# Kernel optimization log

Hardware: AMD Instinct MI355X
Metric: run time of the kernel (lower is better)

## Reference

```python
import jax, jax.numpy as jnp
import numpy as np

BS, MA, H, NH = 64, 64, 64, 4  # molecules, max atoms per molecule, hsize, n_heads


def _lengths():
    # deterministic ragged molecule sizes in [24, 64]
    return np.array([24 + (7 * i) % 41 for i in range(BS)], dtype=np.int64)


def _scopes():
    lengths = _lengths()
    N = int(lengths.sum())  # 2774
    scope = np.zeros((BS, MA), dtype=np.int64)      # pad slots gather row 0 (zeros)
    rev = np.zeros((N,), dtype=np.int64)            # flat atom -> b*MA + slot
    pos = 1                                          # flat row 0 is the zero pad row
    for b, L in enumerate(lengths):
        scope[b, :L] = np.arange(pos, pos + L)
        rev[pos - 1:pos - 1 + L] = b * MA + np.arange(L)
        pos += L
    return scope, rev, N


def setup_inputs() -> dict:
    key = jax.random.key(0)
    k0, k1, k2, k3 = jax.random.split(key, 4)
    scope, rev, N = _scopes()
    inputs = jax.random.normal(k0, (N + 1, H), dtype=jnp.float32)
    inputs = inputs.at[0].set(0.0)  # zero pad row, as in graphretro flat tensors
    Wa_pair = jax.random.normal(k1, (H, H * NH), dtype=jnp.float32) * (1.0 / np.sqrt(H))
    Wa_score = jax.random.normal(k2, (H, NH), dtype=jnp.float32) * (1.0 / np.sqrt(H))
    W_proj = jax.random.normal(k3, (H * NH, H), dtype=jnp.float32) * (1.0 / np.sqrt(H * NH))
    return {
        "inputs": inputs,
        "scope_tensor": jnp.asarray(scope),
        "scope_rev_tensor": jnp.asarray(rev),
        "Wa_pair": Wa_pair,
        "Wa_score": Wa_score,
        "W_proj": W_proj,
    }


def reference(inputs, scope_tensor, scope_rev_tensor, Wa_pair, Wa_score, W_proj):
    bs, ma = scope_tensor.shape
    h = inputs.shape[1]
    nh = Wa_score.shape[1]
    # flat_to_batch: [bs, ma, h]; pad slots pull the zero row 0
    c_batch = inputs[scope_tensor]
    # get_pair: pairwise sum of atom embeddings -> [bs, ma, ma, h]
    atom_pair = c_batch[:, :, None, :] + c_batch[:, None, :, :]
    # Wa_pair (no bias) + relu, viewed as [bs, ma, ma, h, nh]
    total_att = jax.nn.relu(atom_pair @ Wa_pair).reshape(bs, ma, ma, h, nh)
    # einsum '...hn,hjn->...jn' with j==1, then sigmoid -> [bs, ma, ma, nh]
    att_score = jax.nn.sigmoid(jnp.einsum('bijhn,hn->bijn', total_att, Wa_score))
    # att_score * c_atom[b,j,h], summed over j -> [bs, ma, h, nh]
    c_sum = jnp.einsum('bijn,bjh->bihn', att_score, c_batch)
    # view to [bs, ma, h*nh] (h-major, matching torch .view) and project
    c_atom_att = c_sum.reshape(bs, ma, h * nh) @ W_proj  # [bs, ma, h]
    c_mol_att = c_atom_att.sum(axis=1)  # [bs, h]
    # batch_to_flat + prepend zero row -> [N+1, h]
    flat = c_atom_att.reshape(bs * ma, h)[scope_rev_tensor]
    c_atom_att_flat = jnp.concatenate([jnp.zeros((1, h), flat.dtype), flat], axis=0)
    return (c_mol_att, c_atom_att_flat)
```

## Files before the change

### kernel.cpp

```cpp
#include <hip/hip_runtime.h>
#include <stdint.h>

typedef _Float16 h2 __attribute__((ext_vector_type(2)));
typedef _Float16 h8 __attribute__((ext_vector_type(8)));
typedef float f32x4 __attribute__((ext_vector_type(4)));
typedef unsigned int u32;
typedef unsigned short u16;

#define WT_STR 68
#define PJ_STR 68
#define WP_STR 268
#define PI_STR 36
#define CB_STR 72
#define CT_STR 68
#define AB_STR 72
#define CS_STR 264
#define WS_STR 36

__device__ __forceinline__ u32 pk2(float a, float b) {
    return __builtin_bit_cast(u32, __builtin_amdgcn_cvt_pkrtz(a, b));
}
__device__ __forceinline__ h8 frag4(u32 a, u32 b, u32 c, u32 d) {
    return __builtin_bit_cast(h8, make_uint4(a, b, c, d));
}

__global__ __launch_bounds__(512, 1) void atom_attn(
    const float* __restrict__ inputs,
    const int*   __restrict__ scope,
    const float* __restrict__ Wa_pair,
    const float* __restrict__ Wa_score,
    const float* __restrict__ W_proj,
    float* __restrict__ out_mol,
    float* __restrict__ out_flat)
{
    __shared__ __align__(16) u16 s_wa[256 * WT_STR];
    __shared__ __align__(16) u16 s_pj[256 * PJ_STR];
    __shared__ __align__(16) u16 s_wp[64 * WP_STR];
    __shared__ __align__(16) u32 s_pi[4 * 16 * PI_STR];
    __shared__ __align__(16) u16 s_cb[64 * CB_STR];
    __shared__ __align__(16) u16 s_ct[64 * CT_STR];
    __shared__ __align__(16) u16 s_ab[64 * AB_STR];
    __shared__ __align__(16) u16 s_cs[16 * CS_STR];
    __shared__ __align__(16) u32 s_ws[4 * WS_STR];

    const int t = threadIdx.x;
    const int w = t >> 6, l = t & 63;
    const int ml = l & 15, q = l >> 4;
    const int b = blockIdx.y, bx = blockIdx.x;
    const int i_base = bx * 16;

    if (t < 256) {
        if (t < 128) {
            const int n = t & 3, hh = t >> 2;
            const float g0 = Wa_score[(2 * hh) * 4 + n];
            const float g1 = Wa_score[(2 * hh + 1) * 4 + n];
            s_ws[n * WS_STR + hh] = pk2(g0, g1);
        }
        {
            const int jp = (t & 31) * 2;
            const int pp = t >> 5;
            const int r0 = scope[b * 64 + jp];
            const int r1 = scope[b * 64 + jp + 1];
            const f32x4 a0 = *(const f32x4*)(inputs + (size_t)r0 * 64 + pp * 8);
            const f32x4 a1 = *(const f32x4*)(inputs + (size_t)r0 * 64 + pp * 8 + 4);
            const f32x4 b0 = *(const f32x4*)(inputs + (size_t)r1 * 64 + pp * 8);
            const f32x4 b1 = *(const f32x4*)(inputs + (size_t)r1 * 64 + pp * 8 + 4);
            float A[8] = {a0[0], a0[1], a0[2], a0[3], a1[0], a1[1], a1[2], a1[3]};
            float B[8] = {b0[0], b0[1], b0[2], b0[3], b1[0], b1[1], b1[2], b1[3]};
            *(uint4*)&s_cb[jp * CB_STR + pp * 8] =
                make_uint4(pk2(A[0], A[1]), pk2(A[2], A[3]), pk2(A[4], A[5]), pk2(A[6], A[7]));
            *(uint4*)&s_cb[(jp + 1) * CB_STR + pp * 8] =
                make_uint4(pk2(B[0], B[1]), pk2(B[2], B[3]), pk2(B[4], B[5]), pk2(B[6], B[7]));
            #pragma unroll
            for (int e = 0; e < 8; ++e)
                *(u32*)&s_ct[(pp * 8 + e) * CT_STR + jp] = pk2(A[e], B[e]);
        }
        {
            const int o0 = (t & 31) * 2, seg = t >> 5;
            #pragma unroll
            for (int k2 = 0; k2 < 16; ++k2) {
                const int c0 = seg * 32 + k2 * 2;
                const float2 r0 = *(const float2*)(W_proj + c0 * 64 + o0);
                const float2 r1 = *(const float2*)(W_proj + (c0 + 1) * 64 + o0);
                *(u32*)&s_wp[o0 * WP_STR + c0]       = pk2(r0.x, r1.x);
                *(u32*)&s_wp[(o0 + 1) * WP_STR + c0] = pk2(r0.y, r1.y);
            }
        }
    } else {
        const int t2 = t & 255;
        const int cg = (t2 & 127) * 2;
        const int hh2 = t2 >> 7;
        const int cp0 = (cg & 3) * 64 + (cg >> 2);
        #pragma unroll
        for (int k2 = 0; k2 < 16; ++k2) {
            const int h0 = hh2 * 32 + k2 * 2;
            const float2 r0 = *(const float2*)(Wa_pair + h0 * 256 + cg);
            const float2 r1 = *(const float2*)(Wa_pair + (h0 + 1) * 256 + cg);
            *(u32*)&s_wa[cp0 * WT_STR + h0]        = pk2(r0.x, r1.x);
            *(u32*)&s_wa[(cp0 + 64) * WT_STR + h0] = pk2(r0.y, r1.y);
        }
    }
    __syncthreads();

    {
        const int mq = w & 3, jh = w >> 2;
        f32x4 D[4][2];
        #pragma unroll
        for (int k = 0; k < 4; ++k) { D[k][0] = (f32x4)0.f; D[k][1] = (f32x4)0.f; }
        h8 bf[2][2];
        #pragma unroll
        for (int jt = 0; jt < 2; ++jt)
            #pragma unroll
            for (int ks = 0; ks < 2; ++ks)
                bf[jt][ks] = __builtin_bit_cast(h8,
                    *(const uint4*)&s_cb[((jh * 2 + jt) * 16 + ml) * CB_STR + ks * 32 + q * 8]);
        #pragma unroll
        for (int k = 0; k < 4; ++k) {
            const int mt = mq * 4 + k;
            #pragma unroll
            for (int ks = 0; ks < 2; ++ks) {
                const uint2 x0 = *(const uint2*)&s_wa[(mt * 16 + ml) * WT_STR + ks * 32 + q * 8];
                const uint2 x1 = *(const uint2*)&s_wa[(mt * 16 + ml) * WT_STR + ks * 32 + q * 8 + 4];
                const h8 af = frag4(x0.x, x0.y, x1.x, x1.y);
                D[k][0] = __builtin_amdgcn_mfma_f32_16x16x32_f16(af, bf[0][ks], D[k][0], 0, 0, 0);
                D[k][1] = __builtin_amdgcn_mfma_f32_16x16x32_f16(af, bf[1][ks], D[k][1], 0, 0, 0);
            }
        }
        #pragma unroll
        for (int k = 0; k < 4; ++k) {
            const int mt = mq * 4 + k;
            const int nb = mt >> 2, h0 = (mt & 3) * 16 + q * 4;
            #pragma unroll
            for (int jt = 0; jt < 2; ++jt) {
                const int jtile = jh * 2 + jt;
                const int j = jtile * 16 + ml;
                const u32 p0 = pk2(D[k][jt][0], D[k][jt][1]);
                const u32 p1 = pk2(D[k][jt][2], D[k][jt][3]);
                *(uint2*)&s_pj[(nb * 64 + j) * PJ_STR + h0] = make_uint2(p0, p1);
                if (jtile == bx)
                    *(uint2*)&s_pi[(nb * 16 + ml) * PI_STR + (h0 >> 1)] = make_uint2(p0, p1);
            }
        }
    }
    __syncthreads();

    {
        const int n = w & 3, ih = w >> 2;
        u32 pj_u[32];
        #pragma unroll
        for (int k = 0; k < 16; ++k) {
            const uint2 v = *(const uint2*)&s_pj[(n * 64 + l) * PJ_STR + k * 4];
            pj_u[2 * k] = v.x; pj_u[2 * k + 1] = v.y;
        }
        u32 ws_u[32];
        #pragma unroll
        for (int k = 0; k < 8; ++k) {
            const uint4 v = *(const uint4*)&s_ws[n * WS_STR + k * 4];
            ws_u[4 * k] = v.x; ws_u[4 * k + 1] = v.y; ws_u[4 * k + 2] = v.z; ws_u[4 * k + 3] = v.w;
        }
        const h2 zero2 = {(_Float16)0.f, (_Float16)0.f};
        #pragma unroll
        for (int ii = 0; ii < 8; ++ii) {
            const int iloc = ih * 8 + ii;
            const u32* pir = &s_pi[(n * 16 + iloc) * PI_STR];
            float s0 = 0.f, s1 = 0.f;
            #pragma unroll
            for (int c8 = 0; c8 < 8; ++c8) {
                const uint4 pv = *(const uint4*)&pir[c8 * 4];
                const u32 pe[4] = {pv.x, pv.y, pv.z, pv.w};
                #pragma unroll
                for (int e = 0; e < 4; ++e) {
                    const h2 pi2 = __builtin_bit_cast(h2, pe[e]);
                    const h2 pj2 = __builtin_bit_cast(h2, pj_u[c8 * 4 + e]);
                    h2 tv = pi2 + pj2;
                    tv = __builtin_elementwise_max(tv, zero2);
                    if (e & 1)
                        s1 = __builtin_amdgcn_fdot2(tv,
                                __builtin_bit_cast(h2, ws_u[c8 * 4 + e]), s1, false);
                    else
                        s0 = __builtin_amdgcn_fdot2(tv,
                                __builtin_bit_cast(h2, ws_u[c8 * 4 + e]), s0, false);
                }
            }
            const float s = s0 + s1;
            const float a = 1.f / (1.f + __expf(-s));
            const _Float16 ah = (_Float16)a;
            s_ab[(iloc * 4 + n) * AB_STR + l] = __builtin_bit_cast(u16, ah);
        }
    }
    __syncthreads();

    {
        const int mt3 = w & 3, nh = w >> 2;
        h8 af3[2];
        #pragma unroll
        for (int ks = 0; ks < 2; ++ks)
            af3[ks] = __builtin_bit_cast(h8,
                *(const uint4*)&s_ab[(mt3 * 16 + ml) * AB_STR + ks * 32 + q * 8]);
        #pragma unroll
        for (int nx = 0; nx < 2; ++nx) {
            const int nt = nh * 2 + nx;
            f32x4 D2 = (f32x4)0.f;
            #pragma unroll
            for (int ks = 0; ks < 2; ++ks) {
                const uint2 y0 = *(const uint2*)&s_ct[(nt * 16 + ml) * CT_STR + ks * 32 + q * 8];
                const uint2 y1 = *(const uint2*)&s_ct[(nt * 16 + ml) * CT_STR + ks * 32 + q * 8 + 4];
                const h8 bfc = frag4(y0.x, y0.y, y1.x, y1.y);
                D2 = __builtin_amdgcn_mfma_f32_16x16x32_f16(af3[ks], bfc, D2, 0, 0, 0);
            }
            const int iloc = mt3 * 4 + q, h = nt * 16 + ml;
            *(uint2*)&s_cs[iloc * CS_STR + h * 4] =
                make_uint2(pk2(D2[0], D2[1]), pk2(D2[2], D2[3]));
        }
    }
    __syncthreads();

    if (w < 4) {
        f32x4 D4 = (f32x4)0.f;
        #pragma unroll
        for (int ks = 0; ks < 8; ++ks) {
            const h8 af = __builtin_bit_cast(h8,
                *(const uint4*)&s_cs[ml * CS_STR + ks * 32 + q * 8]);
            const uint2 z0 = *(const uint2*)&s_wp[(w * 16 + ml) * WP_STR + ks * 32 + q * 8];
            const uint2 z1 = *(const uint2*)&s_wp[(w * 16 + ml) * WP_STR + ks * 32 + q * 8 + 4];
            const h8 bf4 = frag4(z0.x, z0.y, z1.x, z1.y);
            D4 = __builtin_amdgcn_mfma_f32_16x16x32_f16(af, bf4, D4, 0, 0, 0);
        }
        const int o = w * 16 + ml;
        #pragma unroll
        for (int r = 0; r < 4; ++r) {
            const int iloc = q * 4 + r;
            const int row = scope[b * 64 + i_base + iloc];
            if (row > 0) out_flat[(size_t)row * 64 + o] = D4[r];
        }
        float s4 = D4[0] + D4[1] + D4[2] + D4[3];
        s4 += __shfl_xor(s4, 16, 64);
        s4 += __shfl_xor(s4, 32, 64);
        if (l < 16) atomicAdd(out_mol + b * 64 + o, s4);
    }
}

extern "C" void kernel_launch(void* const* d_in, const int* in_sizes, int n_in,
                              void* d_out, int out_size, void* d_ws, size_t ws_size,
                              hipStream_t stream) {
    const float* inputs   = (const float*)d_in[0];
    const int*   scope    = (const int*)d_in[1];
    const float* Wa_pair  = (const float*)d_in[3];
    const float* Wa_score = (const float*)d_in[4];
    const float* W_proj   = (const float*)d_in[5];
    float* out = (float*)d_out;

    (void)hipMemsetAsync(d_out, 0, (64 * 64 + 64) * sizeof(float), stream);

    dim3 grid(4, 64);
    atom_attn<<<grid, 512, 0, stream>>>(inputs, scope, Wa_pair, Wa_score,
                                        W_proj, out, out + 64 * 64);
}
```

Measured before the change: 74.88 us.

## Prepack weights in separate kernel and split each molecule across eight blocks

Adds a small pack_weights kernel that converts Wa_pair, W_proj and Wa_score to fp16 in MFMA-fragment order in workspace, so the main kernel loads weight fragments straight into registers instead of transposing them into shared memory in every block. The main grid doubles to eight blocks per molecule, each handling 8 query atoms, with shared memory cut and launch bounds raised to allow more resident blocks. The trade-offs are an extra kernel launch, redundant recomputation of the per-molecule pair projection in twice as many blocks, and zero-padded rows in the final projection MFMA.

```diff
diff --git a/kernel.cpp b/kernel.cpp
--- a/kernel.cpp
+++ b/kernel.cpp
@@ -7,15 +7,12 @@
 typedef unsigned int u32;
 typedef unsigned short u16;
 
-#define WT_STR 68
 #define PJ_STR 68
-#define WP_STR 268
 #define PI_STR 36
 #define CB_STR 72
 #define CT_STR 68
 #define AB_STR 72
 #define CS_STR 264
-#define WS_STR 36
 
 __device__ __forceinline__ u32 pk2(float a, float b) {
     return __builtin_bit_cast(u32, __builtin_amdgcn_cvt_pkrtz(a, b));
@@ -24,86 +21,97 @@
     return __builtin_bit_cast(h8, make_uint4(a, b, c, d));
 }
 
-__global__ __launch_bounds__(512, 1) void atom_attn(
-    const float* __restrict__ inputs,
-    const int*   __restrict__ scope,
+__global__ __launch_bounds__(256) void pack_weights(
     const float* __restrict__ Wa_pair,
     const float* __restrict__ Wa_score,
     const float* __restrict__ W_proj,
+    u32* __restrict__ wpk)
+{
+    const int g = blockIdx.x * 256 + threadIdx.x;
+    u32 v[4];
+    if (g < 2048) {
+        #pragma unroll
+        for (int k = 0; k < 4; ++k) {
+            const int idx = g * 4 + k;
+            const int cp = idx >> 5, hh = idx & 31;
+            const int c = (cp & 63) * 4 + (cp >> 6);
+            v[k] = pk2(Wa_pair[(2 * hh) * 256 + c], Wa_pair[(2 * hh + 1) * 256 + c]);
+        }
+        *(uint4*)(wpk + g * 4) = make_uint4(v[0], v[1], v[2], v[3]);
+    } else {
+        #pragma unroll
+        for (int k = 0; k < 4; ++k) {
+            const int idx = (g - 2048) * 4 + k;
+            const int o = idx >> 7, cc = idx & 127;
+            v[k] = pk2(W_proj[(2 * cc) * 64 + o], W_proj[(2 * cc + 1) * 64 + o]);
+        }
+        *(uint4*)(wpk + 8192 + (g - 2048) * 4) = make_uint4(v[0], v[1], v[2], v[3]);
+    }
+    if (g < 128) {
+        const int n = g & 3, hh = g >> 2;
+        wpk[16384 + n * 32 + hh] =
+            pk2(Wa_score[(2 * hh) * 4 + n], Wa_score[(2 * hh + 1) * 4 + n]);
+    }
+}
+
+__global__ __launch_bounds__(512, 4) void atom_attn(
+    const float* __restrict__ inputs,
+    const int*   __restrict__ scope,
+    const u32*   __restrict__ wpk,
     float* __restrict__ out_mol,
     float* __restrict__ out_flat)
 {
-    __shared__ __align__(16) u16 s_wa[256 * WT_STR];
     __shared__ __align__(16) u16 s_pj[256 * PJ_STR];
-    __shared__ __align__(16) u16 s_wp[64 * WP_STR];
-    __shared__ __align__(16) u32 s_pi[4 * 16 * PI_STR];
+    __shared__ __align__(16) u32 s_pi[4 * 8 * PI_STR];
     __shared__ __align__(16) u16 s_cb[64 * CB_STR];
     __shared__ __align__(16) u16 s_ct[64 * CT_STR];
-    __shared__ __align__(16) u16 s_ab[64 * AB_STR];
+    __shared__ __align__(16) u16 s_ab[32 * AB_STR];
     __shared__ __align__(16) u16 s_cs[16 * CS_STR];
-    __shared__ __align__(16) u32 s_ws[4 * WS_STR];
+
+    const u32* __restrict__ waT = wpk;
+    const u32* __restrict__ wpT = wpk + 8192;
+    const u32* __restrict__ wsg = wpk + 16384;
 
     const int t = threadIdx.x;
     const int w = t >> 6, l = t & 63;
     const int ml = l & 15, q = l >> 4;
     const int b = blockIdx.y, bx = blockIdx.x;
-    const int i_base = bx * 16;
+    const int i_base = bx * 8;
+
+    const int mq = w & 3, jh = w >> 2;
+    uint4 afr[4][2];
+    #pragma unroll
+    for (int k = 0; k < 4; ++k)
+        #pragma unroll
+        for (int ks = 0; ks < 2; ++ks)
+            afr[k][ks] = *(const uint4*)(waT + ((mq * 4 + k) * 16 + ml) * 32 + ks * 16 + q * 4);
 
     if (t < 256) {
-        if (t < 128) {
-            const int n = t & 3, hh = t >> 2;
-            const float g0 = Wa_score[(2 * hh) * 4 + n];
-            const float g1 = Wa_score[(2 * hh + 1) * 4 + n];
-            s_ws[n * WS_STR + hh] = pk2(g0, g1);
-        }
-        {
-            const int jp = (t & 31) * 2;
-            const int pp = t >> 5;
-            const int r0 = scope[b * 64 + jp];
-            const int r1 = scope[b * 64 + jp + 1];
-            const f32x4 a0 = *(const f32x4*)(inputs + (size_t)r0 * 64 + pp * 8);
-            const f32x4 a1 = *(const f32x4*)(inputs + (size_t)r0 * 64 + pp * 8 + 4);
-            const f32x4 b0 = *(const f32x4*)(inputs + (size_t)r1 * 64 + pp * 8);
-            const f32x4 b1 = *(const f32x4*)(inputs + (size_t)r1 * 64 + pp * 8 + 4);
-            float A[8] = {a0[0], a0[1], a0[2], a0[3], a1[0], a1[1], a1[2], a1[3]};
-            float B[8] = {b0[0], b0[1], b0[2], b0[3], b1[0], b1[1], b1[2], b1[3]};
-            *(uint4*)&s_cb[jp * CB_STR + pp * 8] =
-                make_uint4(pk2(A[0], A[1]), pk2(A[2], A[3]), pk2(A[4], A[5]), pk2(A[6], A[7]));
-            *(uint4*)&s_cb[(jp + 1) * CB_STR + pp * 8] =
-                make_uint4(pk2(B[0], B[1]), pk2(B[2], B[3]), pk2(B[4], B[5]), pk2(B[6], B[7]));
-            #pragma unroll
-            for (int e = 0; e < 8; ++e)
-                *(u32*)&s_ct[(pp * 8 + e) * CT_STR + jp] = pk2(A[e], B[e]);
-        }
-        {
-            const int o0 = (t & 31) * 2, seg = t >> 5;
-            #pragma unroll
-            for (int k2 = 0; k2 < 16; ++k2) {
-                const int c0 = seg * 32 + k2 * 2;
-                const float2 r0 = *(const float2*)(W_proj + c0 * 64 + o0);
-                const float2 r1 = *(const float2*)(W_proj + (c0 + 1) * 64 + o0);
-                *(u32*)&s_wp[o0 * WP_STR + c0]       = pk2(r0.x, r1.x);
-                *(u32*)&s_wp[(o0 + 1) * WP_STR + c0] = pk2(r0.y, r1.y);
-            }
-        }
-    } else {
-        const int t2 = t & 255;
-        const int cg = (t2 & 127) * 2;
-        const int hh2 = t2 >> 7;
-        const int cp0 = (cg & 3) * 64 + (cg >> 2);
-        #pragma unroll
-        for (int k2 = 0; k2 < 16; ++k2) {
-            const int h0 = hh2 * 32 + k2 * 2;
-            const float2 r0 = *(const float2*)(Wa_pair + h0 * 256 + cg);
-            const float2 r1 = *(const float2*)(Wa_pair + (h0 + 1) * 256 + cg);
-            *(u32*)&s_wa[cp0 * WT_STR + h0]        = pk2(r0.x, r1.x);
-            *(u32*)&s_wa[(cp0 + 64) * WT_STR + h0] = pk2(r0.y, r1.y);
-        }
-    }
-    __syncthreads();
-
-    {
-        const int mq = w & 3, jh = w >> 2;
+        const int jp = (t & 31) * 2;
+        const int pp = t >> 5;
+        const int r0 = scope[b * 64 + jp];
+        const int r1 = scope[b * 64 + jp + 1];
+        const f32x4 a0 = *(const f32x4*)(inputs + (size_t)r0 * 64 + pp * 8);
+        const f32x4 a1 = *(const f32x4*)(inputs + (size_t)r0 * 64 + pp * 8 + 4);
+        const f32x4 b0 = *(const f32x4*)(inputs + (size_t)r1 * 64 + pp * 8);
+        const f32x4 b1 = *(const f32x4*)(inputs + (size_t)r1 * 64 + pp * 8 + 4);
+        float A[8] = {a0[0], a0[1], a0[2], a0[3], a1[0], a1[1], a1[2], a1[3]};
+        float B[8] = {b0[0], b0[1], b0[2], b0[3], b1[0], b1[1], b1[2], b1[3]};
+        *(uint4*)&s_cb[jp * CB_STR + pp * 8] =
+            make_uint4(pk2(A[0], A[1]), pk2(A[2], A[3]), pk2(A[4], A[5]), pk2(A[6], A[7]));
+        *(uint4*)&s_cb[(jp + 1) * CB_STR + pp * 8] =
+            make_uint4(pk2(B[0], B[1]), pk2(B[2], B[3]), pk2(B[4], B[5]), pk2(B[6], B[7]));
+        #pragma unroll
+        for (int e = 0; e < 8; ++e)
+            *(u32*)&s_ct[(pp * 8 + e) * CT_STR + jp] = pk2(A[e], B[e]);
+    }
+    {
+        u32* z = (u32*)(s_cs + 8 * CS_STR);
+        for (int idx = t; idx < 1056; idx += 512) z[idx] = 0;
+    }
+    __syncthreads();
+
+    {
         f32x4 D[4][2];
         #pragma unroll
         for (int k = 0; k < 4; ++k) { D[k][0] = (f32x4)0.f; D[k][1] = (f32x4)0.f; }
@@ -116,12 +124,9 @@
                     *(const uint4*)&s_cb[((jh * 2 + jt) * 16 + ml) * CB_STR + ks * 32 + q * 8]);
         #pragma unroll
         for (int k = 0; k < 4; ++k) {
-            const int mt = mq * 4 + k;
             #pragma unroll
             for (int ks = 0; ks < 2; ++ks) {
-                const uint2 x0 = *(const uint2*)&s_wa[(mt * 16 + ml) * WT_STR + ks * 32 + q * 8];
-                const uint2 x1 = *(const uint2*)&s_wa[(mt * 16 + ml) * WT_STR + ks * 32 + q * 8 + 4];
-                const h8 af = frag4(x0.x, x0.y, x1.x, x1.y);
+                const h8 af = __builtin_bit_cast(h8, afr[k][ks]);
                 D[k][0] = __builtin_amdgcn_mfma_f32_16x16x32_f16(af, bf[0][ks], D[k][0], 0, 0, 0);
                 D[k][1] = __builtin_amdgcn_mfma_f32_16x16x32_f16(af, bf[1][ks], D[k][1], 0, 0, 0);
             }
@@ -137,8 +142,8 @@
                 const u32 p0 = pk2(D[k][jt][0], D[k][jt][1]);
                 const u32 p1 = pk2(D[k][jt][2], D[k][jt][3]);
                 *(uint2*)&s_pj[(nb * 64 + j) * PJ_STR + h0] = make_uint2(p0, p1);
-                if (jtile == bx)
-                    *(uint2*)&s_pi[(nb * 16 + ml) * PI_STR + (h0 >> 1)] = make_uint2(p0, p1);
+                if (jtile == (bx >> 1) && ((ml >> 3) == (bx & 1)))
+                    *(uint2*)&s_pi[(nb * 8 + (ml & 7)) * PI_STR + (h0 >> 1)] = make_uint2(p0, p1);
             }
         }
     }
@@ -149,20 +154,21 @@
         u32 pj_u[32];
         #pragma unroll
         for (int k = 0; k < 16; ++k) {
-            const uint2 v = *(const uint2*)&s_pj[(n * 64 + l) * PJ_STR + k * 4];
-            pj_u[2 * k] = v.x; pj_u[2 * k + 1] = v.y;
+            const uint2 vv = *(const uint2*)&s_pj[(n * 64 + l) * PJ_STR + k * 4];
+            pj_u[2 * k] = vv.x; pj_u[2 * k + 1] = vv.y;
         }
         u32 ws_u[32];
         #pragma unroll
         for (int k = 0; k < 8; ++k) {
-            const uint4 v = *(const uint4*)&s_ws[n * WS_STR + k * 4];
-            ws_u[4 * k] = v.x; ws_u[4 * k + 1] = v.y; ws_u[4 * k + 2] = v.z; ws_u[4 * k + 3] = v.w;
+            const uint4 vv = *(const uint4*)(wsg + n * 32 + k * 4);
+            ws_u[4 * k] = vv.x; ws_u[4 * k + 1] = vv.y;
+            ws_u[4 * k + 2] = vv.z; ws_u[4 * k + 3] = vv.w;
         }
         const h2 zero2 = {(_Float16)0.f, (_Float16)0.f};
         #pragma unroll
-        for (int ii = 0; ii < 8; ++ii) {
-            const int iloc = ih * 8 + ii;
-            const u32* pir = &s_pi[(n * 16 + iloc) * PI_STR];
+        for (int ii = 0; ii < 4; ++ii) {
+            const int iloc = ih * 4 + ii;
+            const u32* pir = &s_pi[(n * 8 + iloc) * PI_STR];
             float s0 = 0.f, s1 = 0.f;
             #pragma unroll
             for (int c8 = 0; c8 < 8; ++c8) {
@@ -190,28 +196,31 @@
     }
     __syncthreads();
 
-    {
-        const int mt3 = w & 3, nh = w >> 2;
+    uint4 wfr[8];
+    if (w < 4) {
+        #pragma unroll
+        for (int ks = 0; ks < 8; ++ks)
+            wfr[ks] = *(const uint4*)(wpT + (w * 16 + ml) * 128 + ks * 16 + q * 4);
+    }
+
+    {
+        const int mt3 = w & 1, nt = w >> 1;
         h8 af3[2];
         #pragma unroll
         for (int ks = 0; ks < 2; ++ks)
             af3[ks] = __builtin_bit_cast(h8,
                 *(const uint4*)&s_ab[(mt3 * 16 + ml) * AB_STR + ks * 32 + q * 8]);
-        #pragma unroll
-        for (int nx = 0; nx < 2; ++nx) {
-            const int nt = nh * 2 + nx;
-            f32x4 D2 = (f32x4)0.f;
-            #pragma unroll
-            for (int ks = 0; ks < 2; ++ks) {
-                const uint2 y0 = *(const uint2*)&s_ct[(nt * 16 + ml) * CT_STR + ks * 32 + q * 8];
-                const uint2 y1 = *(const uint2*)&s_ct[(nt * 16 + ml) * CT_STR + ks * 32 + q * 8 + 4];
-                const h8 bfc = frag4(y0.x, y0.y, y1.x, y1.y);
-                D2 = __builtin_amdgcn_mfma_f32_16x16x32_f16(af3[ks], bfc, D2, 0, 0, 0);
-            }
-            const int iloc = mt3 * 4 + q, h = nt * 16 + ml;
-            *(uint2*)&s_cs[iloc * CS_STR + h * 4] =
-                make_uint2(pk2(D2[0], D2[1]), pk2(D2[2], D2[3]));
-        }
+        f32x4 D2 = (f32x4)0.f;
+        #pragma unroll
+        for (int ks = 0; ks < 2; ++ks) {
+            const uint2 y0 = *(const uint2*)&s_ct[(nt * 16 + ml) * CT_STR + ks * 32 + q * 8];
+            const uint2 y1 = *(const uint2*)&s_ct[(nt * 16 + ml) * CT_STR + ks * 32 + q * 8 + 4];
+            const h8 bfc = frag4(y0.x, y0.y, y1.x, y1.y);
+            D2 = __builtin_amdgcn_mfma_f32_16x16x32_f16(af3[ks], bfc, D2, 0, 0, 0);
+        }
+        const int iloc = mt3 * 4 + q, h = nt * 16 + ml;
+        *(uint2*)&s_cs[iloc * CS_STR + h * 4] =
+            make_uint2(pk2(D2[0], D2[1]), pk2(D2[2], D2[3]));
     }
     __syncthreads();
 
@@ -221,17 +230,17 @@
         for (int ks = 0; ks < 8; ++ks) {
             const h8 af = __builtin_bit_cast(h8,
                 *(const uint4*)&s_cs[ml * CS_STR + ks * 32 + q * 8]);
-            const uint2 z0 = *(const uint2*)&s_wp[(w * 16 + ml) * WP_STR + ks * 32 + q * 8];
-            const uint2 z1 = *(const uint2*)&s_wp[(w * 16 + ml) * WP_STR + ks * 32 + q * 8 + 4];
-            const h8 bf4 = frag4(z0.x, z0.y, z1.x, z1.y);
-            D4 = __builtin_amdgcn_mfma_f32_16x16x32_f16(af, bf4, D4, 0, 0, 0);
+            D4 = __builtin_amdgcn_mfma_f32_16x16x32_f16(af, __builtin_bit_cast(h8, wfr[ks]),
+                                                        D4, 0, 0, 0);
         }
         const int o = w * 16 + ml;
         #pragma unroll
         for (int r = 0; r < 4; ++r) {
             const int iloc = q * 4 + r;
-            const int row = scope[b * 64 + i_base + iloc];
-            if (row > 0) out_flat[(size_t)row * 64 + o] = D4[r];
+            if (iloc < 8) {
+                const int row = scope[b * 64 + i_base + iloc];
+                if (row > 0) out_flat[(size_t)row * 64 + o] = D4[r];
+            }
         }
         float s4 = D4[0] + D4[1] + D4[2] + D4[3];
         s4 += __shfl_xor(s4, 16, 64);
@@ -249,10 +258,12 @@
     const float* Wa_score = (const float*)d_in[4];
     const float* W_proj   = (const float*)d_in[5];
     float* out = (float*)d_out;
+    u32* wpk = (u32*)d_ws;
 
     (void)hipMemsetAsync(d_out, 0, (64 * 64 + 64) * sizeof(float), stream);
 
-    dim3 grid(4, 64);
-    atom_attn<<<grid, 512, 0, stream>>>(inputs, scope, Wa_pair, Wa_score,
-                                        W_proj, out, out + 64 * 64);
-}
+    pack_weights<<<dim3(16), 256, 0, stream>>>(Wa_pair, Wa_score, W_proj, wpk);
+
+    dim3 grid(8, 64);
+    atom_attn<<<grid, 512, 0, stream>>>(inputs, scope, wpk, out, out + 64 * 64);
+}
```

New measurement: 78.81 us. 5.2% more time.

## Split work per head and pre-project atoms through W_proj before attention sum

Applied to the files above, without the earlier changes.

Each block now handles one attention head for a whole molecule instead of a 16-row slice across all heads. The projection is reassociated: atom embeddings are multiplied by each head's W_proj slice before the attention-weighted sum, which removes the separate c_sum staging and the final projection stage. The four heads' partial outputs are combined with atomic adds into out_flat, so the whole output is now zeroed with a memset. This trades one synchronisation stage and much smaller shared memory for many more global float atomics on the flat output.

```diff
diff --git a/kernel.cpp b/kernel.cpp
--- a/kernel.cpp
+++ b/kernel.cpp
@@ -7,15 +7,12 @@
 typedef unsigned int u32;
 typedef unsigned short u16;
 
-#define WT_STR 68
-#define PJ_STR 68
-#define WP_STR 268
-#define PI_STR 36
 #define CB_STR 72
-#define CT_STR 68
+#define WA_STR 68
+#define WP_STR 68
+#define P_STR  68
+#define CW_STR 68
 #define AB_STR 72
-#define CS_STR 264
-#define WS_STR 36
 
 __device__ __forceinline__ u32 pk2(float a, float b) {
     return __builtin_bit_cast(u32, __builtin_amdgcn_cvt_pkrtz(a, b));
@@ -33,141 +30,131 @@
     float* __restrict__ out_mol,
     float* __restrict__ out_flat)
 {
-    __shared__ __align__(16) u16 s_wa[256 * WT_STR];
-    __shared__ __align__(16) u16 s_pj[256 * PJ_STR];
+    __shared__ __align__(16) u16 s_cb[64 * CB_STR];
+    __shared__ __align__(16) u16 s_wa[64 * WA_STR];
     __shared__ __align__(16) u16 s_wp[64 * WP_STR];
-    __shared__ __align__(16) u32 s_pi[4 * 16 * PI_STR];
-    __shared__ __align__(16) u16 s_cb[64 * CB_STR];
-    __shared__ __align__(16) u16 s_ct[64 * CT_STR];
+    __shared__ __align__(16) u16 s_p [64 * P_STR ];
+    __shared__ __align__(16) u16 s_cw[64 * CW_STR];
     __shared__ __align__(16) u16 s_ab[64 * AB_STR];
-    __shared__ __align__(16) u16 s_cs[16 * CS_STR];
-    __shared__ __align__(16) u32 s_ws[4 * WS_STR];
+    __shared__ __align__(16) u32 s_ws[32];
 
     const int t = threadIdx.x;
     const int w = t >> 6, l = t & 63;
     const int ml = l & 15, q = l >> 4;
-    const int b = blockIdx.y, bx = blockIdx.x;
-    const int i_base = bx * 16;
+    const int n = blockIdx.x;
+    const int b = blockIdx.y;
 
     if (t < 256) {
-        if (t < 128) {
-            const int n = t & 3, hh = t >> 2;
-            const float g0 = Wa_score[(2 * hh) * 4 + n];
-            const float g1 = Wa_score[(2 * hh + 1) * 4 + n];
-            s_ws[n * WS_STR + hh] = pk2(g0, g1);
-        }
-        {
-            const int jp = (t & 31) * 2;
-            const int pp = t >> 5;
-            const int r0 = scope[b * 64 + jp];
-            const int r1 = scope[b * 64 + jp + 1];
-            const f32x4 a0 = *(const f32x4*)(inputs + (size_t)r0 * 64 + pp * 8);
-            const f32x4 a1 = *(const f32x4*)(inputs + (size_t)r0 * 64 + pp * 8 + 4);
-            const f32x4 b0 = *(const f32x4*)(inputs + (size_t)r1 * 64 + pp * 8);
-            const f32x4 b1 = *(const f32x4*)(inputs + (size_t)r1 * 64 + pp * 8 + 4);
-            float A[8] = {a0[0], a0[1], a0[2], a0[3], a1[0], a1[1], a1[2], a1[3]};
-            float B[8] = {b0[0], b0[1], b0[2], b0[3], b1[0], b1[1], b1[2], b1[3]};
-            *(uint4*)&s_cb[jp * CB_STR + pp * 8] =
-                make_uint4(pk2(A[0], A[1]), pk2(A[2], A[3]), pk2(A[4], A[5]), pk2(A[6], A[7]));
-            *(uint4*)&s_cb[(jp + 1) * CB_STR + pp * 8] =
-                make_uint4(pk2(B[0], B[1]), pk2(B[2], B[3]), pk2(B[4], B[5]), pk2(B[6], B[7]));
-            #pragma unroll
-            for (int e = 0; e < 8; ++e)
-                *(u32*)&s_ct[(pp * 8 + e) * CT_STR + jp] = pk2(A[e], B[e]);
-        }
-        {
-            const int o0 = (t & 31) * 2, seg = t >> 5;
-            #pragma unroll
-            for (int k2 = 0; k2 < 16; ++k2) {
-                const int c0 = seg * 32 + k2 * 2;
-                const float2 r0 = *(const float2*)(W_proj + c0 * 64 + o0);
-                const float2 r1 = *(const float2*)(W_proj + (c0 + 1) * 64 + o0);
-                *(u32*)&s_wp[o0 * WP_STR + c0]       = pk2(r0.x, r1.x);
-                *(u32*)&s_wp[(o0 + 1) * WP_STR + c0] = pk2(r0.y, r1.y);
-            }
+        const int jp = (t & 31) * 2;
+        const int pp = t >> 5;
+        const int r0 = scope[b * 64 + jp];
+        const int r1 = scope[b * 64 + jp + 1];
+        const f32x4 a0 = *(const f32x4*)(inputs + (size_t)r0 * 64 + pp * 8);
+        const f32x4 a1 = *(const f32x4*)(inputs + (size_t)r0 * 64 + pp * 8 + 4);
+        const f32x4 b0 = *(const f32x4*)(inputs + (size_t)r1 * 64 + pp * 8);
+        const f32x4 b1 = *(const f32x4*)(inputs + (size_t)r1 * 64 + pp * 8 + 4);
+        *(uint4*)&s_cb[jp * CB_STR + pp * 8] =
+            make_uint4(pk2(a0[0], a0[1]), pk2(a0[2], a0[3]), pk2(a1[0], a1[1]), pk2(a1[2], a1[3]));
+        *(uint4*)&s_cb[(jp + 1) * CB_STR + pp * 8] =
+            make_uint4(pk2(b0[0], b0[1]), pk2(b0[2], b0[3]), pk2(b1[0], b1[1]), pk2(b1[2], b1[3]));
+    }
+    {
+        float a[8];
+        #pragma unroll
+        for (int e = 0; e < 8; ++e)
+            a[e] = Wa_pair[(w * 8 + e) * 256 + 4 * l + n];
+        *(uint4*)&s_wa[l * WA_STR + w * 8] =
+            make_uint4(pk2(a[0], a[1]), pk2(a[2], a[3]), pk2(a[4], a[5]), pk2(a[6], a[7]));
+    }
+    {
+        u32 v[4];
+        #pragma unroll
+        for (int e = 0; e < 4; ++e) {
+            const int hh = w * 4 + e;
+            const float v0 = W_proj[(8 * hh + n) * 64 + l];
+            const float v1 = W_proj[(8 * hh + 4 + n) * 64 + l];
+            v[e] = pk2(v0, v1);
+        }
+        *(uint4*)&s_wp[l * WP_STR + w * 8] = make_uint4(v[0], v[1], v[2], v[3]);
+    }
+    if (t < 32) {
+        s_ws[t] = pk2(Wa_score[(2 * t) * 4 + n], Wa_score[(2 * t + 1) * 4 + n]);
+    }
+    __syncthreads();
+
+    if (w < 4) {
+        f32x4 D[4];
+        #pragma unroll
+        for (int jt = 0; jt < 4; ++jt) D[jt] = (f32x4)0.f;
+        #pragma unroll
+        for (int ks = 0; ks < 2; ++ks) {
+            const uint2 x0 = *(const uint2*)&s_wa[(w * 16 + ml) * WA_STR + ks * 32 + q * 8];
+            const uint2 x1 = *(const uint2*)&s_wa[(w * 16 + ml) * WA_STR + ks * 32 + q * 8 + 4];
+            const h8 af = frag4(x0.x, x0.y, x1.x, x1.y);
+            #pragma unroll
+            for (int jt = 0; jt < 4; ++jt) {
+                const h8 bf = __builtin_bit_cast(h8,
+                    *(const uint4*)&s_cb[(jt * 16 + ml) * CB_STR + ks * 32 + q * 8]);
+                D[jt] = __builtin_amdgcn_mfma_f32_16x16x32_f16(af, bf, D[jt], 0, 0, 0);
+            }
+        }
+        #pragma unroll
+        for (int jt = 0; jt < 4; ++jt) {
+            const int j = jt * 16 + ml;
+            *(uint2*)&s_p[j * P_STR + w * 16 + q * 4] =
+                make_uint2(pk2(D[jt][0], D[jt][1]), pk2(D[jt][2], D[jt][3]));
         }
     } else {
-        const int t2 = t & 255;
-        const int cg = (t2 & 127) * 2;
-        const int hh2 = t2 >> 7;
-        const int cp0 = (cg & 3) * 64 + (cg >> 2);
-        #pragma unroll
-        for (int k2 = 0; k2 < 16; ++k2) {
-            const int h0 = hh2 * 32 + k2 * 2;
-            const float2 r0 = *(const float2*)(Wa_pair + h0 * 256 + cg);
-            const float2 r1 = *(const float2*)(Wa_pair + (h0 + 1) * 256 + cg);
-            *(u32*)&s_wa[cp0 * WT_STR + h0]        = pk2(r0.x, r1.x);
-            *(u32*)&s_wa[(cp0 + 64) * WT_STR + h0] = pk2(r0.y, r1.y);
+        const int w4 = w - 4;
+        f32x4 D[4];
+        #pragma unroll
+        for (int ot = 0; ot < 4; ++ot) D[ot] = (f32x4)0.f;
+        #pragma unroll
+        for (int ks = 0; ks < 2; ++ks) {
+            const h8 af = __builtin_bit_cast(h8,
+                *(const uint4*)&s_cb[(w4 * 16 + ml) * CB_STR + ks * 32 + q * 8]);
+            #pragma unroll
+            for (int ot = 0; ot < 4; ++ot) {
+                const uint2 y0 = *(const uint2*)&s_wp[(ot * 16 + ml) * WP_STR + ks * 32 + q * 8];
+                const uint2 y1 = *(const uint2*)&s_wp[(ot * 16 + ml) * WP_STR + ks * 32 + q * 8 + 4];
+                const h8 bf = frag4(y0.x, y0.y, y1.x, y1.y);
+                D[ot] = __builtin_amdgcn_mfma_f32_16x16x32_f16(af, bf, D[ot], 0, 0, 0);
+            }
+        }
+        #pragma unroll
+        for (int ot = 0; ot < 4; ++ot) {
+            const int o = ot * 16 + ml;
+            *(uint2*)&s_cw[o * CW_STR + w4 * 16 + q * 4] =
+                make_uint2(pk2(D[ot][0], D[ot][1]), pk2(D[ot][2], D[ot][3]));
         }
     }
     __syncthreads();
 
     {
-        const int mq = w & 3, jh = w >> 2;
-        f32x4 D[4][2];
-        #pragma unroll
-        for (int k = 0; k < 4; ++k) { D[k][0] = (f32x4)0.f; D[k][1] = (f32x4)0.f; }
-        h8 bf[2][2];
-        #pragma unroll
-        for (int jt = 0; jt < 2; ++jt)
-            #pragma unroll
-            for (int ks = 0; ks < 2; ++ks)
-                bf[jt][ks] = __builtin_bit_cast(h8,
-                    *(const uint4*)&s_cb[((jh * 2 + jt) * 16 + ml) * CB_STR + ks * 32 + q * 8]);
-        #pragma unroll
-        for (int k = 0; k < 4; ++k) {
-            const int mt = mq * 4 + k;
-            #pragma unroll
-            for (int ks = 0; ks < 2; ++ks) {
-                const uint2 x0 = *(const uint2*)&s_wa[(mt * 16 + ml) * WT_STR + ks * 32 + q * 8];
-                const uint2 x1 = *(const uint2*)&s_wa[(mt * 16 + ml) * WT_STR + ks * 32 + q * 8 + 4];
-                const h8 af = frag4(x0.x, x0.y, x1.x, x1.y);
-                D[k][0] = __builtin_amdgcn_mfma_f32_16x16x32_f16(af, bf[0][ks], D[k][0], 0, 0, 0);
-                D[k][1] = __builtin_amdgcn_mfma_f32_16x16x32_f16(af, bf[1][ks], D[k][1], 0, 0, 0);
-            }
-        }
-        #pragma unroll
-        for (int k = 0; k < 4; ++k) {
-            const int mt = mq * 4 + k;
-            const int nb = mt >> 2, h0 = (mt & 3) * 16 + q * 4;
-            #pragma unroll
-            for (int jt = 0; jt < 2; ++jt) {
-                const int jtile = jh * 2 + jt;
-                const int j = jtile * 16 + ml;
-                const u32 p0 = pk2(D[k][jt][0], D[k][jt][1]);
-                const u32 p1 = pk2(D[k][jt][2], D[k][jt][3]);
-                *(uint2*)&s_pj[(nb * 64 + j) * PJ_STR + h0] = make_uint2(p0, p1);
-                if (jtile == bx)
-                    *(uint2*)&s_pi[(nb * 16 + ml) * PI_STR + (h0 >> 1)] = make_uint2(p0, p1);
-            }
-        }
-    }
-    __syncthreads();
-
-    {
-        const int n = w & 3, ih = w >> 2;
         u32 pj_u[32];
         #pragma unroll
         for (int k = 0; k < 16; ++k) {
-            const uint2 v = *(const uint2*)&s_pj[(n * 64 + l) * PJ_STR + k * 4];
-            pj_u[2 * k] = v.x; pj_u[2 * k + 1] = v.y;
+            const uint2 vv = *(const uint2*)&s_p[l * P_STR + k * 4];
+            pj_u[2 * k] = vv.x; pj_u[2 * k + 1] = vv.y;
         }
         u32 ws_u[32];
         #pragma unroll
         for (int k = 0; k < 8; ++k) {
-            const uint4 v = *(const uint4*)&s_ws[n * WS_STR + k * 4];
-            ws_u[4 * k] = v.x; ws_u[4 * k + 1] = v.y; ws_u[4 * k + 2] = v.z; ws_u[4 * k + 3] = v.w;
+            const uint4 vv = *(const uint4*)&s_ws[k * 4];
+            ws_u[4 * k] = vv.x; ws_u[4 * k + 1] = vv.y;
+            ws_u[4 * k + 2] = vv.z; ws_u[4 * k + 3] = vv.w;
         }
         const h2 zero2 = {(_Float16)0.f, (_Float16)0.f};
         #pragma unroll
         for (int ii = 0; ii < 8; ++ii) {
-            const int iloc = ih * 8 + ii;
-            const u32* pir = &s_pi[(n * 16 + iloc) * PI_STR];
+            const int i = w * 8 + ii;
+            const u16* pir = &s_p[i * P_STR];
             float s0 = 0.f, s1 = 0.f;
             #pragma unroll
             for (int c8 = 0; c8 < 8; ++c8) {
-                const uint4 pv = *(const uint4*)&pir[c8 * 4];
-                const u32 pe[4] = {pv.x, pv.y, pv.z, pv.w};
+                const uint2 u0 = *(const uint2*)&pir[c8 * 8];
+                const uint2 u1 = *(const uint2*)&pir[c8 * 8 + 4];
+                const u32 pe[4] = {u0.x, u0.y, u1.x, u1.y};
                 #pragma unroll
                 for (int e = 0; e < 4; ++e) {
                     const h2 pi2 = __builtin_bit_cast(h2, pe[e]);
@@ -185,58 +172,42 @@
             const float s = s0 + s1;
             const float a = 1.f / (1.f + __expf(-s));
             const _Float16 ah = (_Float16)a;
-            s_ab[(iloc * 4 + n) * AB_STR + l] = __builtin_bit_cast(u16, ah);
+            s_ab[i * AB_STR + l] = __builtin_bit_cast(u16, ah);
         }
     }
     __syncthreads();
 
     {
-        const int mt3 = w & 3, nh = w >> 2;
+        const int mt = w & 3, nh2 = w >> 2;
         h8 af3[2];
         #pragma unroll
         for (int ks = 0; ks < 2; ++ks)
             af3[ks] = __builtin_bit_cast(h8,
-                *(const uint4*)&s_ab[(mt3 * 16 + ml) * AB_STR + ks * 32 + q * 8]);
+                *(const uint4*)&s_ab[(mt * 16 + ml) * AB_STR + ks * 32 + q * 8]);
         #pragma unroll
         for (int nx = 0; nx < 2; ++nx) {
-            const int nt = nh * 2 + nx;
-            f32x4 D2 = (f32x4)0.f;
+            const int nt = nh2 * 2 + nx;
+            f32x4 D = (f32x4)0.f;
             #pragma unroll
             for (int ks = 0; ks < 2; ++ks) {
-                const uint2 y0 = *(const uint2*)&s_ct[(nt * 16 + ml) * CT_STR + ks * 32 + q * 8];
-                const uint2 y1 = *(const uint2*)&s_ct[(nt * 16 + ml) * CT_STR + ks * 32 + q * 8 + 4];
-                const h8 bfc = frag4(y0.x, y0.y, y1.x, y1.y);
-                D2 = __builtin_amdgcn_mfma_f32_16x16x32_f16(af3[ks], bfc, D2, 0, 0, 0);
-            }
-            const int iloc = mt3 * 4 + q, h = nt * 16 + ml;
-            *(uint2*)&s_cs[iloc * CS_STR + h * 4] =
-                make_uint2(pk2(D2[0], D2[1]), pk2(D2[2], D2[3]));
-        }
-    }
-    __syncthreads();
-
-    if (w < 4) {
-        f32x4 D4 = (f32x4)0.f;
-        #pragma unroll
-        for (int ks = 0; ks < 8; ++ks) {
-            const h8 af = __builtin_bit_cast(h8,
-                *(const uint4*)&s_cs[ml * CS_STR + ks * 32 + q * 8]);
-            const uint2 z0 = *(const uint2*)&s_wp[(w * 16 + ml) * WP_STR + ks * 32 + q * 8];
-            const uint2 z1 = *(const uint2*)&s_wp[(w * 16 + ml) * WP_STR + ks * 32 + q * 8 + 4];
-            const h8 bf4 = frag4(z0.x, z0.y, z1.x, z1.y);
-            D4 = __builtin_amdgcn_mfma_f32_16x16x32_f16(af, bf4, D4, 0, 0, 0);
-        }
-        const int o = w * 16 + ml;
-        #pragma unroll
-        for (int r = 0; r < 4; ++r) {
-            const int iloc = q * 4 + r;
-            const int row = scope[b * 64 + i_base + iloc];
-            if (row > 0) out_flat[(size_t)row * 64 + o] = D4[r];
-        }
-        float s4 = D4[0] + D4[1] + D4[2] + D4[3];
-        s4 += __shfl_xor(s4, 16, 64);
-        s4 += __shfl_xor(s4, 32, 64);
-        if (l < 16) atomicAdd(out_mol + b * 64 + o, s4);
+                const uint2 y0 = *(const uint2*)&s_cw[(nt * 16 + ml) * CW_STR + ks * 32 + q * 8];
+                const uint2 y1 = *(const uint2*)&s_cw[(nt * 16 + ml) * CW_STR + ks * 32 + q * 8 + 4];
+                const h8 bf = frag4(y0.x, y0.y, y1.x, y1.y);
+                D = __builtin_amdgcn_mfma_f32_16x16x32_f16(af3[ks], bf, D, 0, 0, 0);
+            }
+            const int o = nt * 16 + ml;
+            float colsum = 0.f;
+            #pragma unroll
+            for (int r = 0; r < 4; ++r) {
+                const int i = mt * 16 + q * 4 + r;
+                const int row = scope[b * 64 + i];
+                if (row > 0) atomicAdd(out_flat + (size_t)row * 64 + o, D[r]);
+                colsum += D[r];
+            }
+            colsum += __shfl_xor(colsum, 16, 64);
+            colsum += __shfl_xor(colsum, 32, 64);
+            if (q == 0) atomicAdd(out_mol + b * 64 + o, colsum);
+        }
     }
 }
 
@@ -250,7 +221,7 @@
     const float* W_proj   = (const float*)d_in[5];
     float* out = (float*)d_out;
 
-    (void)hipMemsetAsync(d_out, 0, (64 * 64 + 64) * sizeof(float), stream);
+    (void)hipMemsetAsync(d_out, 0, (size_t)out_size, stream);
 
     dim3 grid(4, 64);
     atom_attn<<<grid, 512, 0, stream>>>(inputs, scope, Wa_pair, Wa_score,
```

New measurement: 75.02 us. Within noise of the previous version (+0.2%).
